# Performance work log

Hardware: AMD Instinct MI355X
Metric: run time of the kernel (lower is better)

The kernel has to match this reference:

```python
import jax, jax.numpy as jnp
import numpy as np

GROUP_SIZE = 7  # init kwarg group_size


def setup_inputs() -> dict:
    key = jax.random.key(0)
    B, D, G, H, W = 2, 8, GROUP_SIZE, 50, 84
    C = D * G * G  # 392
    stride = 16
    N = 128
    k1, k2, k3 = jax.random.split(key, 3)
    features = jax.random.normal(k1, (B, C, H, W), dtype=jnp.float32)
    batch_idx = jax.random.randint(k2, (N,), 0, B).astype(jnp.float32)
    u = jax.random.uniform(k3, (N, 4), dtype=jnp.float32)
    img_w, img_h = float(W * stride), float(H * stride)
    x1 = u[:, 0] * (img_w * 0.5)
    y1 = u[:, 1] * (img_h * 0.5)
    x2 = x1 + u[:, 2] * (img_w * 0.45) + 16.0
    y2 = y1 + u[:, 3] * (img_h * 0.45) + 16.0
    rois = jnp.stack([batch_idx, x1, y1, x2, y2], axis=1)  # [N,5]
    return {"rois": rois, "features": features, "stride": stride}


def _bin_masks(rois, scale, G, H, W, dtype):
    # R-FCN PSRoI pooling bin geometry (rounded roi corners, end+1).
    xs = jnp.round(rois[:, 1]) * scale
    ys = jnp.round(rois[:, 2]) * scale
    xe = (jnp.round(rois[:, 3]) + 1.0) * scale
    ye = (jnp.round(rois[:, 4]) + 1.0) * scale
    bin_w = jnp.maximum(xe - xs, 0.1) / G  # [N]
    bin_h = jnp.maximum(ye - ys, 0.1) / G
    g = jnp.arange(G, dtype=dtype)
    wstart = jnp.clip(jnp.floor(g[None, :] * bin_w[:, None] + xs[:, None]), 0, W)  # [N,G]
    wend = jnp.clip(jnp.ceil((g[None, :] + 1.0) * bin_w[:, None] + xs[:, None]), 0, W)
    hstart = jnp.clip(jnp.floor(g[None, :] * bin_h[:, None] + ys[:, None]), 0, H)
    hend = jnp.clip(jnp.ceil((g[None, :] + 1.0) * bin_h[:, None] + ys[:, None]), 0, H)
    wgrid = jnp.arange(W, dtype=dtype)
    hgrid = jnp.arange(H, dtype=dtype)
    mask_w = ((wgrid[None, None, :] >= wstart[:, :, None]) &
              (wgrid[None, None, :] < wend[:, :, None])).astype(dtype)   # [N,G,W]
    mask_h = ((hgrid[None, None, :] >= hstart[:, :, None]) &
              (hgrid[None, None, :] < hend[:, :, None])).astype(dtype)   # [N,G,H]
    # bin area; empty bins have zero-sum masks so dividing by max(area,1) yields 0
    area = jnp.maximum((hend - hstart)[:, :, None] * (wend - wstart)[:, None, :], 1.0)  # [N,Gh,Gw]
    return mask_h, mask_w, area


def reference(rois, features, stride):
    G = GROUP_SIZE
    scale = 1.0 / float(stride)
    B, C, H, W = features.shape
    D = C // (G * G)
    rois = rois[:, :5].astype(features.dtype)
    batch_idx = rois[:, 0].astype(jnp.int32)  # [N]
    mask_h, mask_w, area = _bin_masks(rois, scale, G, H, W, features.dtype)
    # position-sensitive channel mapping: channel c = (d*G + i)*G + j
    featr = features.reshape(B, D, G, G, H, W)[batch_idx]  # [N,D,Gh,Gw,H,W]
    pooled = jnp.einsum('ndijhw,nih,njw->ndij', featr, mask_h, mask_w)
    return pooled / area[:, None, :, :]  # [N, D, G, G]
```

## Files before the change

kernel.cpp:

```cpp
#include <hip/hip_runtime.h>


#define GS 7
#define DD 8
#define BB 2
#define HH 50
#define WW 84

__global__ void psroi_kernel(const float* __restrict__ rois,
                             const float* __restrict__ feat,
                             const int*   __restrict__ stride_ptr,
                             float*       __restrict__ out,
                             int total) {
    #pragma clang fp contract(off)

    int idx = blockIdx.x * blockDim.x + threadIdx.x;
    if (idx >= total) return;

    int j = idx % GS;
    int i = (idx / GS) % GS;
    int d = (idx / (GS * GS)) % DD;
    int n = idx / (GS * GS * DD);

    float scale = 1.0f / (float)(*stride_ptr);

    const float* r = rois + (size_t)n * 5;

    int b = (int)r[0];
    b = b < 0 ? 0 : (b > (BB - 1) ? (BB - 1) : b);

    float xs = rintf(r[1]) * scale;
    float ys = rintf(r[2]) * scale;
    float xe = (rintf(r[3]) + 1.0f) * scale;
    float ye = (rintf(r[4]) + 1.0f) * scale;

    const float rcp7 = 1.0f / 7.0f;
    float bin_w = fmaxf(xe - xs, 0.1f) * rcp7;
    float bin_h = fmaxf(ye - ys, 0.1f) * rcp7;

    float jf = (float)j;
    float fi = (float)i;

    float wstart = fminf(fmaxf(floorf(jf * bin_w + xs), 0.0f), (float)WW);
    float wend   = fminf(fmaxf(ceilf((jf + 1.0f) * bin_w + xs), 0.0f), (float)WW);
    float hstart = fminf(fmaxf(floorf(fi * bin_h + ys), 0.0f), (float)HH);
    float hend   = fminf(fmaxf(ceilf((fi + 1.0f) * bin_h + ys), 0.0f), (float)HH);

    float area = fmaxf((hend - hstart) * (wend - wstart), 1.0f);

    int hs = (int)hstart, he = (int)hend;
    int ws = (int)wstart, we = (int)wend;

    int c = (d * GS + i) * GS + j;
    const float* fbase = feat + ((size_t)b * (DD * GS * GS) + c) * (HH * WW);

    float sum = 0.0f;
    for (int h = hs; h < he; ++h) {
        const float* row = fbase + (size_t)h * WW;
        for (int w = ws; w < we; ++w) {
            sum += row[w];
        }
    }

    out[idx] = sum / area;
}

extern "C" void kernel_launch(void* const* d_in, const int* in_sizes, int n_in,
                              void* d_out, int out_size, void* d_ws, size_t ws_size,
                              hipStream_t stream) {
    const float* rois   = (const float*)d_in[0];
    const float* feat   = (const float*)d_in[1];
    const int*   stride = (const int*)d_in[2];
    float*       out    = (float*)d_out;

    int total = out_size;
    int block = 256;
    int grid  = (total + block - 1) / block;
    psroi_kernel<<<grid, block, 0, stream>>>(rois, feat, stride, out, total);
}
```

Measured before the change: 73.73 us.

## Split each pooling bin across 8 lanes with shuffle reduction

Each output bin is now summed by 8 threads, arranged as 2 rows by 4 columns of the bin's window, and the partial sums are combined with xor shuffles. This exposes more parallelism and shortens the serial accumulation loop that dominated each thread in the original kernel. The cost is 8x more threads, redundant geometry computation per lane, and a different floating-point summation order.

```diff
diff --git a/kernel.cpp b/kernel.cpp
--- a/kernel.cpp
+++ b/kernel.cpp
@@ -11,16 +11,18 @@
                              const float* __restrict__ feat,
                              const int*   __restrict__ stride_ptr,
                              float*       __restrict__ out,
-                             int total) {
+                             int nbins) {
     #pragma clang fp contract(off)
 
-    int idx = blockIdx.x * blockDim.x + threadIdx.x;
-    if (idx >= total) return;
+    int t = blockIdx.x * blockDim.x + threadIdx.x;
+    int bin  = t >> 3;
+    int lane = t & 7;
+    if (bin >= nbins) return;
 
-    int j = idx % GS;
-    int i = (idx / GS) % GS;
-    int d = (idx / (GS * GS)) % DD;
-    int n = idx / (GS * GS * DD);
+    int j = bin % GS;
+    int i = (bin / GS) % GS;
+    int d = (bin / (GS * GS)) % DD;
+    int n = bin / (GS * GS * DD);
 
     float scale = 1.0f / (float)(*stride_ptr);
 
@@ -54,15 +56,22 @@
     int c = (d * GS + i) * GS + j;
     const float* fbase = feat + ((size_t)b * (DD * GS * GS) + c) * (HH * WW);
 
+    int lh = lane >> 2;
+    int lw = lane & 3;
+
     float sum = 0.0f;
-    for (int h = hs; h < he; ++h) {
+    for (int h = hs + lh; h < he; h += 2) {
         const float* row = fbase + (size_t)h * WW;
-        for (int w = ws; w < we; ++w) {
+        for (int w = ws + lw; w < we; w += 4) {
             sum += row[w];
         }
     }
 
-    out[idx] = sum / area;
+    sum += __shfl_xor(sum, 1, 64);
+    sum += __shfl_xor(sum, 2, 64);
+    sum += __shfl_xor(sum, 4, 64);
+
+    if (lane == 0) out[bin] = sum / area;
 }
 
 extern "C" void kernel_launch(void* const* d_in, const int* in_sizes, int n_in,
@@ -73,8 +82,9 @@
     const int*   stride = (const int*)d_in[2];
     float*       out    = (float*)d_out;
 
-    int total = out_size;
+    int nbins = out_size;
+    int threads = nbins * 8;
     int block = 256;
-    int grid  = (total + block - 1) / block;
-    psroi_kernel<<<grid, block, 0, stream>>>(rois, feat, stride, out, total);
+    int grid  = (threads + block - 1) / block;
+    psroi_kernel<<<grid, block, 0, stream>>>(rois, feat, stride, out, nbins);
 }
```

After: 67.96 us. -7.8%, faster.
